# Kernel tuning notes

Measured on AMD Instinct MI355X. Metric: run time of the kernel, lower is better.

## Reference

```python
import jax, jax.numpy as jnp
import numpy as np

N = 8192      # num_nodes
B = 16        # batch
IN_DIM = 2    # input_dim
HID = 64      # hid_dim
K = 2         # diffusion_steps
DEG = 16
E = N * DEG
F = IN_DIM + HID            # concat(input, state) feature dim
NUM_MAT = 2 * K + 1         # dual random walk: 2 matrices * K steps + identity


def _spmm(vals, rows, cols, x):
    # sparse [N,N] @ dense [N,M]: y[rows[e]] += vals[e] * x[cols[e]]
    return jax.ops.segment_sum(vals[:, None] * x[cols], rows, num_segments=N)


def _diff_conv(x, W, b, edge_src, edge_dst, vals1, vals2):
    # x: [B, N, F] -> [B, N*out_dim]; Chebyshev-like diffusion recursion
    x0 = jnp.transpose(x, (1, 2, 0)).reshape(N, F * B)  # [N, F*B]
    xs = [x0]
    # matrix 1 = D_out^-1 A (edges src->dst), matrix 2 = D_in^-1 A^T (edges dst->src)
    for rows, cols, vals in ((edge_src, edge_dst, vals1), (edge_dst, edge_src, vals2)):
        x1 = _spmm(vals, rows, cols, x0)
        xs.append(x1)
        xp, xc = x0, x1
        for _ in range(2, K + 1):
            xn = 2.0 * _spmm(vals, rows, cols, xc) - xp
            xs.append(xn)
            xp, xc = xc, xn
    xstk = jnp.stack(xs, 0).reshape(NUM_MAT, N, F, B)
    xstk = jnp.transpose(xstk, (3, 1, 2, 0)).reshape(B * N, F * NUM_MAT)
    out = xstk @ W + b  # [B*N, out_dim]
    return out.reshape(B, -1)


def setup_inputs() -> dict:
    key = jax.random.key(0)
    k = jax.random.split(key, 8)
    inputs = jax.random.normal(k[0], (B, N * IN_DIM), jnp.float32)
    state = jax.random.normal(k[1], (B, N * HID), jnp.float32)
    edge_src = jax.random.randint(k[2], (E,), 0, N)
    edge_dst = jax.random.randint(k[3], (E,), 0, N)
    a = jax.random.uniform(k[4], (E,), jnp.float32) + 0.1  # positive edge weights
    dout = jax.ops.segment_sum(a, edge_src, num_segments=N)
    din = jax.ops.segment_sum(a, edge_dst, num_segments=N)
    vals1 = a / jnp.where(dout > 0, dout, 1.0)[edge_src]  # random-walk normalize A
    vals2 = a / jnp.where(din > 0, din, 1.0)[edge_dst]    # random-walk normalize A^T
    std_g = 1.414 * np.sqrt(2.0 / (F * NUM_MAT + 2 * HID)).astype(np.float32)
    std_c = 1.414 * np.sqrt(2.0 / (F * NUM_MAT + HID)).astype(np.float32)
    W_gate = jax.random.normal(k[5], (F * NUM_MAT, 2 * HID), jnp.float32) * std_g
    b_gate = jnp.zeros((2 * HID,), jnp.float32)
    W_cand = jax.random.normal(k[6], (F * NUM_MAT, HID), jnp.float32) * std_c
    b_cand = jnp.zeros((HID,), jnp.float32)
    return dict(inputs=inputs, state=state, edge_src=edge_src, edge_dst=edge_dst,
                vals1=vals1, vals2=vals2, W_gate=W_gate, b_gate=b_gate,
                W_cand=W_cand, b_cand=b_cand)


def reference(inputs, state, edge_src, edge_dst, vals1, vals2,
              W_gate, b_gate, W_cand, b_cand):
    i = inputs.reshape(B, N, IN_DIM)
    s = state.reshape(B, N, HID)
    x = jnp.concatenate([i, s], axis=2)  # [B, N, F]
    value = jax.nn.sigmoid(_diff_conv(x, W_gate, b_gate, edge_src, edge_dst, vals1, vals2))
    value = value.reshape(B, N, 2 * HID)
    r = value[..., :HID].reshape(B, N * HID)
    u = value[..., HID:].reshape(B, N * HID)
    rs = (r * state).reshape(B, N, HID)
    xc = jnp.concatenate([i, rs], axis=2)
    c = jnp.tanh(_diff_conv(xc, W_cand, b_cand, edge_src, edge_dst, vals1, vals2))
    new_state = u * state + (1.0 - u) * c
    return (new_state, new_state)
```

## Files before the change

### kernel.cpp

```cpp
#include <hip/hip_runtime.h>
#include <cstddef>
#include <cstdint>

#define NNODES 8192
#define BATCH  16
#define HID    64
#define NEDGE  131072
#define SN     524288
#define OUTHALF 8388608
#define FP2    72
#define SLABU  1152
#define NSTR   5760
#define NSTR4  720
#define XCS4   144
#define KP2    384
#define GN     8

typedef __attribute__((ext_vector_type(8))) short bf16x8;
typedef __attribute__((ext_vector_type(4))) float f32x4;

static __device__ __forceinline__ float bf2f(ushort u) {
    union { uint32_t i; float f; } c; c.i = ((uint32_t)u) << 16; return c.f;
}
static __device__ __forceinline__ ushort f2bf(float f) {
    union { float f; uint32_t i; } c; c.f = f;
    uint32_t lsb = (c.i >> 16) & 1;
    return (ushort)((c.i + 0x7fffu + lsb) >> 16);
}


__global__ void zero_counts_kernel(int* __restrict__ c1, int* __restrict__ c2) {
    int i = blockIdx.x * 256 + threadIdx.x;
    if (i < NNODES) { c1[i] = 0; c2[i] = 0; }
}

__global__ void hist_kernel(const int* __restrict__ src, const int* __restrict__ dst,
                            int* __restrict__ c1, int* __restrict__ c2) {
    int e = blockIdx.x * 256 + threadIdx.x;
    if (e < NEDGE) {
        atomicAdd(&c1[src[e]], 1);
        atomicAdd(&c2[dst[e]], 1);
    }
}

__global__ __launch_bounds__(1024) void scan_kernel(const int* __restrict__ counts,
                                                    int* __restrict__ rowptr,
                                                    int* __restrict__ cursor) {
    __shared__ int sh[1024];
    int tid = threadIdx.x;
    int base = tid * 8;
    int local[8];
    int sum = 0;
#pragma unroll
    for (int j = 0; j < 8; ++j) { local[j] = counts[base + j]; sum += local[j]; }
    sh[tid] = sum;
    __syncthreads();
    for (int off = 1; off < 1024; off <<= 1) {
        int v = (tid >= off) ? sh[tid - off] : 0;
        __syncthreads();
        sh[tid] += v;
        __syncthreads();
    }
    int p = sh[tid] - sum;
#pragma unroll
    for (int j = 0; j < 8; ++j) {
        cursor[base + j] = p;
        p += local[j];
        rowptr[base + j + 1] = p;
    }
    if (tid == 0) rowptr[0] = 0;
}

__global__ void scatter_kernel(const int* __restrict__ src, const int* __restrict__ dst,
                               const float* __restrict__ v1, const float* __restrict__ v2,
                               int* __restrict__ cur1, int* __restrict__ cur2,
                               int* __restrict__ cols1, float* __restrict__ valsC1,
                               int* __restrict__ cols2, float* __restrict__ valsC2) {
    int e = blockIdx.x * 256 + threadIdx.x;
    if (e < NEDGE) {
        int r1 = src[e];
        int p1 = atomicAdd(&cur1[r1], 1);
        cols1[p1] = dst[e];
        valsC1[p1] = v1[e];
        int r2 = dst[e];
        int p2 = atomicAdd(&cur2[r2], 1);
        cols2[p2] = src[e];
        valsC2[p2] = v2[e];
    }
}


__global__ void convert_w_kernel(const float* __restrict__ Wg, const float* __restrict__ Wc,
                                 ushort* __restrict__ WgT, ushort* __restrict__ WcT) {
    int i = blockIdx.x * 256 + threadIdx.x;
    if (i >= 192 * KP2) return;
    int col = i / KP2, k2 = i - col * KP2;
    int m = k2 / FP2, f = k2 - m * FP2;
    bool valid = (m < 5) && (f < 66);
    int ko = f * 5 + m;
    if (col < 128) {
        WgT[col * KP2 + k2] = valid ? f2bf(Wg[ko * 128 + col]) : (ushort)0;
    } else {
        int c = col - 128;
        WcT[c * KP2 + k2] = valid ? f2bf(Wc[ko * 64 + c]) : (ushort)0;
    }
}


__global__ void build_x0_kernel(const float* __restrict__ inputs, const float* __restrict__ state,
                                uint* __restrict__ Xb_u, uint* __restrict__ Xc_u) {
    int t = blockIdx.x * 256 + threadIdx.x;
    if (t >= NNODES * BATCH * 36) return;
    int n = t / 576;
    int r = t - n * 576;
    int b = r / 36;
    int j = r - b * 36;
    int f0 = 2 * j;
    uint val = 0;
    if (f0 == 0) {
        float v0 = inputs[(size_t)b * (NNODES * 2) + n * 2 + 0];
        float v1 = inputs[(size_t)b * (NNODES * 2) + n * 2 + 1];
        val = (uint)f2bf(v0) | ((uint)f2bf(v1) << 16);
    } else if (f0 < 66) {
        float v0 = state[(size_t)b * SN + n * HID + (f0 - 2)];
        float v1 = state[(size_t)b * SN + n * HID + (f0 - 1)];
        val = (uint)f2bf(v0) | ((uint)f2bf(v1) << 16);
    }
    Xb_u[(size_t)n * 2880 + r] = val;
    if (f0 == 0 || f0 >= 66) Xc_u[t] = val;
}


static __device__ __forceinline__ void fma8(float* acc, uint4 d, float v) {
    acc[0] += v * bf2f((ushort)(d.x));  acc[1] += v * bf2f((ushort)(d.x >> 16));
    acc[2] += v * bf2f((ushort)(d.y));  acc[3] += v * bf2f((ushort)(d.y >> 16));
    acc[4] += v * bf2f((ushort)(d.z));  acc[5] += v * bf2f((ushort)(d.z >> 16));
    acc[6] += v * bf2f((ushort)(d.w));  acc[7] += v * bf2f((ushort)(d.w >> 16));
}

static __device__ __forceinline__ uint4 blend_pack8(const float* acc, uint4 p,
                                                    float alpha, float beta) {
    float o[8];
    o[0] = alpha * acc[0] + beta * bf2f((ushort)(p.x));
    o[1] = alpha * acc[1] + beta * bf2f((ushort)(p.x >> 16));
    o[2] = alpha * acc[2] + beta * bf2f((ushort)(p.y));
    o[3] = alpha * acc[3] + beta * bf2f((ushort)(p.y >> 16));
    o[4] = alpha * acc[4] + beta * bf2f((ushort)(p.z));
    o[5] = alpha * acc[5] + beta * bf2f((ushort)(p.z >> 16));
    o[6] = alpha * acc[6] + beta * bf2f((ushort)(p.w));
    o[7] = alpha * acc[7] + beta * bf2f((ushort)(p.w >> 16));
    uint4 r;
    r.x = (uint32_t)f2bf(o[0]) | ((uint32_t)f2bf(o[1]) << 16);
    r.y = (uint32_t)f2bf(o[2]) | ((uint32_t)f2bf(o[3]) << 16);
    r.z = (uint32_t)f2bf(o[4]) | ((uint32_t)f2bf(o[5]) << 16);
    r.w = (uint32_t)f2bf(o[6]) | ((uint32_t)f2bf(o[7]) << 16);
    return r;
}

__global__ __launch_bounds__(128) void spmm_kernel(const int* __restrict__ rowptr,
                                                   const int* __restrict__ cols,
                                                   const float* __restrict__ vals,
                                                   const uint4* __restrict__ x, int xs,
                                                   const uint4* __restrict__ xp, int ps,
                                                   uint4* __restrict__ y, int ys,
                                                   float alpha, float beta) {
    int n = blockIdx.x;
    int t = threadIdx.x;
    int s = rowptr[n], e = rowptr[n + 1];
    float a0[8] = {0, 0, 0, 0, 0, 0, 0, 0};
    float a1[8] = {0, 0, 0, 0, 0, 0, 0, 0};
    bool tail = t < 16;
    int t2 = 128 + t;
    int i = s;
    for (; i + 2 <= e; i += 2) {
        int cA = cols[i], cB = cols[i + 1];
        float vA = vals[i], vB = vals[i + 1];
        const uint4* rA = x + (size_t)cA * xs;
        const uint4* rB = x + (size_t)cB * xs;
        uint4 dA = rA[t];
        uint4 dB = rB[t];
        uint4 dA1, dB1;
        if (tail) { dA1 = rA[t2]; dB1 = rB[t2]; }
        fma8(a0, dA, vA); fma8(a0, dB, vB);
        if (tail) { fma8(a1, dA1, vA); fma8(a1, dB1, vB); }
    }
    if (i < e) {
        int cA = cols[i];
        float vA = vals[i];
        const uint4* rA = x + (size_t)cA * xs;
        uint4 dA = rA[t];
        if (tail) { uint4 dA1 = rA[t2]; fma8(a1, dA1, vA); }
        fma8(a0, dA, vA);
    }
    uint4* yb = y + (size_t)n * ys;
    const uint4* xpb = xp + (size_t)n * ps;
    uint4 p0 = (beta != 0.f) ? xpb[t] : make_uint4(0, 0, 0, 0);
    yb[t] = blend_pack8(a0, p0, alpha, beta);
    if (tail) {
        uint4 p1 = (beta != 0.f) ? xpb[t2] : make_uint4(0, 0, 0, 0);
        yb[t2] = blend_pack8(a1, p1, alpha, beta);
    }
}


__global__ __launch_bounds__(256, 2) void gate_mfma(const ushort* __restrict__ Xb,
                                                    const ushort* __restrict__ WgT,
                                                    const float* __restrict__ bg,
                                                    const float* __restrict__ state,
                                                    float* __restrict__ U,
                                                    ushort* __restrict__ Xc) {
    int tid = threadIdx.x;
    int wave = tid >> 6, lane = tid & 63;
    int row = lane & 15, quad = lane >> 4;
    int c0 = wave * 32 + row;
    int c1 = c0 + 16;

    bf16x8 w0[12], w1[12];
#pragma unroll
    for (int kt = 0; kt < 12; ++kt) {
        w0[kt] = *(const bf16x8*)(WgT + (size_t)c0 * KP2 + kt * 32 + quad * 8);
        w1[kt] = *(const bf16x8*)(WgT + (size_t)c1 * KP2 + kt * 32 + quad * 8);
    }
    float bias0 = bg[c0], bias1 = bg[c1];

    int offA[11];
#pragma unroll
    for (int kt = 0; kt < 11; ++kt) {
        int j = 4 * kt + quad;
        int m = j / 9;
        int f0 = 8 * (j - 9 * m);
        offA[kt] = m * SLABU + row * FP2 + f0;
    }
    int off11 = 4 * SLABU + row * FP2 + 64;

    int nodeBase = blockIdx.x * GN;
    for (int g = 0; g < GN; ++g) {
        int n = nodeBase + g;
        const ushort* An = Xb + (size_t)n * NSTR;
        f32x4 acc0 = {0.f, 0.f, 0.f, 0.f};
        f32x4 acc1 = {0.f, 0.f, 0.f, 0.f};
#pragma unroll
        for (int kt = 0; kt < 11; ++kt) {
            bf16x8 av = *(const bf16x8*)(An + offA[kt]);
            acc0 = __builtin_amdgcn_mfma_f32_16x16x32_bf16(av, w0[kt], acc0, 0, 0, 0);
            acc1 = __builtin_amdgcn_mfma_f32_16x16x32_bf16(av, w1[kt], acc1, 0, 0, 0);
        }
        {
            bf16x8 av = {0, 0, 0, 0, 0, 0, 0, 0};
            if (quad == 0) av = *(const bf16x8*)(An + off11);
            acc0 = __builtin_amdgcn_mfma_f32_16x16x32_bf16(av, w0[11], acc0, 0, 0, 0);
            acc1 = __builtin_amdgcn_mfma_f32_16x16x32_bf16(av, w1[11], acc1, 0, 0, 0);
        }
#pragma unroll
        for (int r = 0; r < 4; ++r) {
            int b = quad * 4 + r;
            float v0 = 1.f / (1.f + __expf(-(acc0[r] + bias0)));
            float v1 = 1.f / (1.f + __expf(-(acc1[r] + bias1)));
            if (wave < 2) {
                float s0 = state[(size_t)b * SN + n * HID + c0];
                float s1 = state[(size_t)b * SN + n * HID + c1];
                Xc[(size_t)n * SLABU + b * FP2 + 2 + c0] = f2bf(v0 * s0);
                Xc[(size_t)n * SLABU + b * FP2 + 2 + c1] = f2bf(v1 * s1);
            } else {
                U[(size_t)b * SN + n * HID + (c0 - HID)] = v0;
                U[(size_t)b * SN + n * HID + (c1 - HID)] = v1;
            }
        }
    }
}


__global__ __launch_bounds__(256, 3) void cand_mfma(const ushort* __restrict__ Xb,
                                                    const ushort* __restrict__ Xc,
                                                    const ushort* __restrict__ WcT,
                                                    const float* __restrict__ bc,
                                                    const float* __restrict__ state,
                                                    const float* U,
                                                    float* out) {
    int tid = threadIdx.x;
    int wave = tid >> 6, lane = tid & 63;
    int row = lane & 15, quad = lane >> 4;
    int c = wave * 16 + row;

    bf16x8 w[12];
#pragma unroll
    for (int kt = 0; kt < 12; ++kt)
        w[kt] = *(const bf16x8*)(WcT + (size_t)c * KP2 + kt * 32 + quad * 8);
    float bias = bc[c];

    int offA[11];
#pragma unroll
    for (int kt = 0; kt < 11; ++kt) {
        int j = 4 * kt + quad;
        int m = j / 9;
        int f0 = 8 * (j - 9 * m);
        offA[kt] = m * SLABU + row * FP2 + f0;
    }
    int off11 = 4 * SLABU + row * FP2 + 64;

    int nodeBase = blockIdx.x * GN;
    for (int g = 0; g < GN; ++g) {
        int n = nodeBase + g;
        const ushort* AnB = Xb + (size_t)n * NSTR;
        const ushort* AnC = Xc + (size_t)n * SLABU;
        f32x4 acc = {0.f, 0.f, 0.f, 0.f};
#pragma unroll
        for (int kt = 0; kt < 11; ++kt) {
            const ushort* bp = (kt < 2) ? AnC
                             : (kt == 2 ? (quad == 0 ? AnC : AnB) : AnB);
            bf16x8 av = *(const bf16x8*)(bp + offA[kt]);
            acc = __builtin_amdgcn_mfma_f32_16x16x32_bf16(av, w[kt], acc, 0, 0, 0);
        }
        {
            bf16x8 av = {0, 0, 0, 0, 0, 0, 0, 0};
            if (quad == 0) av = *(const bf16x8*)(AnB + off11);
            acc = __builtin_amdgcn_mfma_f32_16x16x32_bf16(av, w[11], acc, 0, 0, 0);
        }
#pragma unroll
        for (int r = 0; r < 4; ++r) {
            int b = quad * 4 + r;
            float pre = acc[r] + bias;
            float cv = 1.f - 2.f / (__expf(2.f * pre) + 1.f);
            size_t idx = (size_t)b * SN + n * HID + c;
            float uv = U[idx];
            float s = state[idx];
            float ns = uv * s + (1.f - uv) * cv;
            out[idx] = ns;
            out[OUTHALF + idx] = ns;
        }
    }
}


extern "C" void kernel_launch(void* const* d_in, const int* in_sizes, int n_in,
                              void* d_out, int out_size, void* d_ws, size_t ws_size,
                              hipStream_t stream) {
    const float* inputs = (const float*)d_in[0];
    const float* state  = (const float*)d_in[1];
    const int*   esrc   = (const int*)d_in[2];
    const int*   edst   = (const int*)d_in[3];
    const float* v1     = (const float*)d_in[4];
    const float* v2     = (const float*)d_in[5];
    const float* Wg     = (const float*)d_in[6];
    const float* bg     = (const float*)d_in[7];
    const float* Wc     = (const float*)d_in[8];
    const float* bc     = (const float*)d_in[9];
    float* out = (float*)d_out;

    char* ws = (char*)d_ws;
    size_t off = 0;
    auto alloc = [&](size_t bytes) -> void* {
        void* p = ws + off;
        off += (bytes + 255) & ~(size_t)255;
        return p;
    };
    ushort* Xb     = (ushort*)alloc((size_t)NNODES * NSTR * 2);
    ushort* Xc     = (ushort*)alloc((size_t)NNODES * SLABU * 2);
    ushort* WgT    = (ushort*)alloc((size_t)128 * KP2 * 2);
    ushort* WcT    = (ushort*)alloc((size_t)64 * KP2 * 2);
    int*   counts1 = (int*)alloc(NNODES * 4);
    int*   counts2 = (int*)alloc(NNODES * 4);
    int*   rowptr1 = (int*)alloc((NNODES + 1) * 4);
    int*   rowptr2 = (int*)alloc((NNODES + 1) * 4);
    int*   cursor1 = (int*)alloc(NNODES * 4);
    int*   cursor2 = (int*)alloc(NNODES * 4);
    int*   cols1   = (int*)alloc(NEDGE * 4);
    int*   cols2   = (int*)alloc(NEDGE * 4);
    float* valsC1  = (float*)alloc(NEDGE * 4);
    float* valsC2  = (float*)alloc(NEDGE * 4);

    float* U = out + OUTHALF;

    uint4* Xb4 = (uint4*)Xb;
    uint4* Xc4 = (uint4*)Xc;
    auto slab = [&](int m) { return Xb4 + (size_t)m * 144; };

    zero_counts_kernel<<<(NNODES + 255) / 256, 256, 0, stream>>>(counts1, counts2);
    hist_kernel<<<(NEDGE + 255) / 256, 256, 0, stream>>>(esrc, edst, counts1, counts2);
    scan_kernel<<<1, 1024, 0, stream>>>(counts1, rowptr1, cursor1);
    scan_kernel<<<1, 1024, 0, stream>>>(counts2, rowptr2, cursor2);
    scatter_kernel<<<(NEDGE + 255) / 256, 256, 0, stream>>>(esrc, edst, v1, v2,
                                                            cursor1, cursor2,
                                                            cols1, valsC1, cols2, valsC2);

    convert_w_kernel<<<(192 * KP2 + 255) / 256, 256, 0, stream>>>(Wg, Wc, WgT, WcT);
    build_x0_kernel<<<(NNODES * BATCH * 36 + 255) / 256, 256, 0, stream>>>(
        inputs, state, (uint*)Xb, (uint*)Xc);

    spmm_kernel<<<NNODES, 128, 0, stream>>>(rowptr1, cols1, valsC1, slab(0), NSTR4,
                                            slab(0), NSTR4, slab(1), NSTR4, 1.f, 0.f);
    spmm_kernel<<<NNODES, 128, 0, stream>>>(rowptr1, cols1, valsC1, slab(1), NSTR4,
                                            slab(0), NSTR4, slab(2), NSTR4, 2.f, -1.f);
    spmm_kernel<<<NNODES, 128, 0, stream>>>(rowptr2, cols2, valsC2, slab(0), NSTR4,
                                            slab(0), NSTR4, slab(3), NSTR4, 1.f, 0.f);
    spmm_kernel<<<NNODES, 128, 0, stream>>>(rowptr2, cols2, valsC2, slab(3), NSTR4,
                                            slab(0), NSTR4, slab(4), NSTR4, 2.f, -1.f);

    gate_mfma<<<NNODES / GN, 256, 0, stream>>>(Xb, WgT, bg, state, U, Xc);

    spmm_kernel<<<NNODES, 128, 0, stream>>>(rowptr1, cols1, valsC1, Xc4, XCS4,
                                            Xc4, XCS4, slab(1), NSTR4, 1.f, 0.f);
    spmm_kernel<<<NNODES, 128, 0, stream>>>(rowptr1, cols1, valsC1, slab(1), NSTR4,
                                            Xc4, XCS4, slab(2), NSTR4, 2.f, -1.f);
    spmm_kernel<<<NNODES, 128, 0, stream>>>(rowptr2, cols2, valsC2, Xc4, XCS4,
                                            Xc4, XCS4, slab(3), NSTR4, 1.f, 0.f);
    spmm_kernel<<<NNODES, 128, 0, stream>>>(rowptr2, cols2, valsC2, slab(3), NSTR4,
                                            Xc4, XCS4, slab(4), NSTR4, 2.f, -1.f);

    cand_mfma<<<NNODES / GN, 256, 0, stream>>>(Xb, Xc, WcT, bc, state, U, out);
}
```

Baseline: 610.4 us.

## Merge the two random-walk SpMMs into one dual launch and retune MFMA kernels

Both diffusion directions now run in a single spmm_dual launch with a doubled grid, where each block selects matrix 1 or matrix 2 from its block index. This halves the SpMM launch count and gives each launch twice the blocks to fill the GPU. The SpMM inner loop is unrolled to four edges so more gather loads are in flight. The gate and candidate MFMA kernels process fewer nodes per block (GN 8 to 4) and request higher occupancy in launch bounds, which may limit registers available for the cached weight fragments and cause spills.

Measured after the change: 603.5 us. No clear change (-1.1%).

```diff
diff --git a/kernel.cpp b/kernel.cpp
--- a/kernel.cpp
+++ b/kernel.cpp
@@ -14,7 +14,7 @@
 #define NSTR4  720
 #define XCS4   144
 #define KP2    384
-#define GN     8
+#define GN     4
 
 typedef __attribute__((ext_vector_type(8))) short bf16x8;
 typedef __attribute__((ext_vector_type(4))) float f32x4;
@@ -157,14 +157,24 @@
     return r;
 }
 
-__global__ __launch_bounds__(128) void spmm_kernel(const int* __restrict__ rowptr,
-                                                   const int* __restrict__ cols,
-                                                   const float* __restrict__ vals,
-                                                   const uint4* __restrict__ x, int xs,
-                                                   const uint4* __restrict__ xp, int ps,
-                                                   uint4* __restrict__ y, int ys,
-                                                   float alpha, float beta) {
-    int n = blockIdx.x;
+__global__ __launch_bounds__(128) void spmm_dual(
+        const int* __restrict__ rp1, const int* __restrict__ c1, const float* __restrict__ v1,
+        const uint4* __restrict__ x1,
+        const int* __restrict__ rp2, const int* __restrict__ c2, const float* __restrict__ v2,
+        const uint4* __restrict__ x2,
+        int xs,
+        const uint4* __restrict__ xp, int ps,
+        uint4* __restrict__ y1, uint4* __restrict__ y2, int ys,
+        float alpha, float beta) {
+    int bid = blockIdx.x;
+    int half = bid >> 13;
+    int n = bid & 8191;
+    const int* rowptr = half ? rp2 : rp1;
+    const int* cols   = half ? c2 : c1;
+    const float* vals = half ? v2 : v1;
+    const uint4* x    = half ? x2 : x1;
+    uint4* y          = half ? y2 : y1;
+
     int t = threadIdx.x;
     int s = rowptr[n], e = rowptr[n + 1];
     float a0[8] = {0, 0, 0, 0, 0, 0, 0, 0};
@@ -172,19 +182,20 @@
     bool tail = t < 16;
     int t2 = 128 + t;
     int i = s;
-    for (; i + 2 <= e; i += 2) {
-        int cA = cols[i], cB = cols[i + 1];
-        float vA = vals[i], vB = vals[i + 1];
+    for (; i + 4 <= e; i += 4) {
+        int cA = cols[i], cB = cols[i + 1], cC = cols[i + 2], cD = cols[i + 3];
+        float vA = vals[i], vB = vals[i + 1], vC = vals[i + 2], vD = vals[i + 3];
         const uint4* rA = x + (size_t)cA * xs;
         const uint4* rB = x + (size_t)cB * xs;
-        uint4 dA = rA[t];
-        uint4 dB = rB[t];
-        uint4 dA1, dB1;
-        if (tail) { dA1 = rA[t2]; dB1 = rB[t2]; }
-        fma8(a0, dA, vA); fma8(a0, dB, vB);
-        if (tail) { fma8(a1, dA1, vA); fma8(a1, dB1, vB); }
-    }
-    if (i < e) {
+        const uint4* rC = x + (size_t)cC * xs;
+        const uint4* rD = x + (size_t)cD * xs;
+        uint4 dA = rA[t], dB = rB[t], dC = rC[t], dD = rD[t];
+        uint4 eA, eB, eC, eD;
+        if (tail) { eA = rA[t2]; eB = rB[t2]; eC = rC[t2]; eD = rD[t2]; }
+        fma8(a0, dA, vA); fma8(a0, dB, vB); fma8(a0, dC, vC); fma8(a0, dD, vD);
+        if (tail) { fma8(a1, eA, vA); fma8(a1, eB, vB); fma8(a1, eC, vC); fma8(a1, eD, vD); }
+    }
+    for (; i < e; ++i) {
         int cA = cols[i];
         float vA = vals[i];
         const uint4* rA = x + (size_t)cA * xs;
@@ -203,7 +214,7 @@
 }
 
 
-__global__ __launch_bounds__(256, 2) void gate_mfma(const ushort* __restrict__ Xb,
+__global__ __launch_bounds__(256, 4) void gate_mfma(const ushort* __restrict__ Xb,
                                                     const ushort* __restrict__ WgT,
                                                     const float* __restrict__ bg,
                                                     const float* __restrict__ state,
@@ -270,7 +281,7 @@
 }
 
 
-__global__ __launch_bounds__(256, 3) void cand_mfma(const ushort* __restrict__ Xb,
+__global__ __launch_bounds__(256, 4) void cand_mfma(const ushort* __restrict__ Xb,
                                                     const ushort* __restrict__ Xc,
                                                     const ushort* __restrict__ WcT,
                                                     const float* __restrict__ bc,
@@ -387,25 +398,25 @@
     build_x0_kernel<<<(NNODES * BATCH * 36 + 255) / 256, 256, 0, stream>>>(
         inputs, state, (uint*)Xb, (uint*)Xc);
 
-    spmm_kernel<<<NNODES, 128, 0, stream>>>(rowptr1, cols1, valsC1, slab(0), NSTR4,
-                                            slab(0), NSTR4, slab(1), NSTR4, 1.f, 0.f);
-    spmm_kernel<<<NNODES, 128, 0, stream>>>(rowptr1, cols1, valsC1, slab(1), NSTR4,
-                                            slab(0), NSTR4, slab(2), NSTR4, 2.f, -1.f);
-    spmm_kernel<<<NNODES, 128, 0, stream>>>(rowptr2, cols2, valsC2, slab(0), NSTR4,
-                                            slab(0), NSTR4, slab(3), NSTR4, 1.f, 0.f);
-    spmm_kernel<<<NNODES, 128, 0, stream>>>(rowptr2, cols2, valsC2, slab(3), NSTR4,
-                                            slab(0), NSTR4, slab(4), NSTR4, 2.f, -1.f);
+    spmm_dual<<<2 * NNODES, 128, 0, stream>>>(rowptr1, cols1, valsC1, slab(0),
+                                              rowptr2, cols2, valsC2, slab(0), NSTR4,
+                                              slab(0), NSTR4, slab(1), slab(3), NSTR4,
+                                              1.f, 0.f);
+    spmm_dual<<<2 * NNODES, 128, 0, stream>>>(rowptr1, cols1, valsC1, slab(1),
+                                              rowptr2, cols2, valsC2, slab(3), NSTR4,
+                                              slab(0), NSTR4, slab(2), slab(4), NSTR4,
+                                              2.f, -1.f);
 
     gate_mfma<<<NNODES / GN, 256, 0, stream>>>(Xb, WgT, bg, state, U, Xc);
 
-    spmm_kernel<<<NNODES, 128, 0, stream>>>(rowptr1, cols1, valsC1, Xc4, XCS4,
-                                            Xc4, XCS4, slab(1), NSTR4, 1.f, 0.f);
-    spmm_kernel<<<NNODES, 128, 0, stream>>>(rowptr1, cols1, valsC1, slab(1), NSTR4,
-                                            Xc4, XCS4, slab(2), NSTR4, 2.f, -1.f);
-    spmm_kernel<<<NNODES, 128, 0, stream>>>(rowptr2, cols2, valsC2, Xc4, XCS4,
-                                            Xc4, XCS4, slab(3), NSTR4, 1.f, 0.f);
-    spmm_kernel<<<NNODES, 128, 0, stream>>>(rowptr2, cols2, valsC2, slab(3), NSTR4,
-                                            Xc4, XCS4, slab(4), NSTR4, 2.f, -1.f);
+    spmm_dual<<<2 * NNODES, 128, 0, stream>>>(rowptr1, cols1, valsC1, Xc4,
+                                              rowptr2, cols2, valsC2, Xc4, XCS4,
+                                              Xc4, XCS4, slab(1), slab(3), NSTR4,
+                                              1.f, 0.f);
+    spmm_dual<<<2 * NNODES, 128, 0, stream>>>(rowptr1, cols1, valsC1, slab(1),
+                                              rowptr2, cols2, valsC2, slab(3), NSTR4,
+                                              Xc4, XCS4, slab(2), slab(4), NSTR4,
+                                              2.f, -1.f);
 
     cand_mfma<<<NNODES / GN, 256, 0, stream>>>(Xb, Xc, WcT, bc, state, U, out);
 }
```
